# Kernel optimization log

Measured on AMD Instinct MI355X. Metric: run time of the kernel, lower is better.

The kernel has to match this reference:

```python
import jax, jax.numpy as jnp
import numpy as np

B, S, HID, NH, MAX_TOKENS = 2, 2048, 2048, 16, 2048
HD = HID // NH

def rotate_half(x):
    x1, x2 = x[..., :x.shape[-1] // 2], x[..., x.shape[-1] // 2:]
    return jnp.concatenate((-x2, x1), axis=-1)

def rope_tables():
    inv_freq = 1.0 / (10000.0 ** (jnp.arange(0, HD, 2, dtype=jnp.float32) / HD))
    t = jnp.arange(MAX_TOKENS, dtype=jnp.float32)
    freqs = jnp.outer(t, inv_freq)                       # [T, HD/2]
    emb = jnp.concatenate((freqs, freqs), axis=-1)       # [T, HD]
    return jnp.cos(emb), jnp.sin(emb)

def setup_inputs() -> dict:
    key = jax.random.key(0)
    ks = jax.random.split(key, 5)
    hidden_states = jax.random.normal(ks[0], (B, S, HID), dtype=jnp.float32)
    # additive causal mask [B, 1, S, S]: 0 on/below diag, large negative above
    neg = jnp.finfo(jnp.float32).min
    causal = jnp.where(jnp.tril(jnp.ones((S, S), dtype=bool)), 0.0, neg)
    attention_mask = jnp.broadcast_to(causal[None, None], (B, 1, S, S)).astype(jnp.float32)
    position_ids = jnp.broadcast_to(jnp.arange(S, dtype=jnp.int32), (B, S))
    scale = 1.0 / np.sqrt(HID)
    Wq = jax.random.normal(ks[1], (HID, HID), dtype=jnp.float32) * scale
    Wk = jax.random.normal(ks[2], (HID, HID), dtype=jnp.float32) * scale
    Wv = jax.random.normal(ks[3], (HID, HID), dtype=jnp.float32) * scale
    Wo = jax.random.normal(ks[4], (HID, HID), dtype=jnp.float32) * scale
    return {"hidden_states": hidden_states, "attention_mask": attention_mask,
            "position_ids": position_ids, "Wq": Wq, "Wk": Wk, "Wv": Wv, "Wo": Wo}

def reference(hidden_states, attention_mask, position_ids, Wq, Wk, Wv, Wo):
    b, s, _ = hidden_states.shape
    def proj(W):  # torch Linear: x @ W.T -> [b, H, s, hd]
        return (hidden_states @ W.T).reshape(b, s, NH, HD).transpose(0, 2, 1, 3)
    q, k, v = proj(Wq), proj(Wk), proj(Wv)
    cos_t, sin_t = rope_tables()
    cos = cos_t[position_ids][:, None]   # [b, 1, s, hd]
    sin = sin_t[position_ids][:, None]
    q = q * cos + rotate_half(q) * sin
    k = k * cos + rotate_half(k) * sin
    scores = jnp.einsum('bhqd,bhkd->bhqk', q, k) / np.sqrt(HD)
    scores = jnp.maximum(scores + attention_mask, jnp.finfo(scores.dtype).min)
    attn = jax.nn.softmax(scores.astype(jnp.float32), axis=-1).astype(q.dtype)
    out = jnp.einsum('bhqk,bhkd->bhqd', attn, v)
    out = out.transpose(0, 2, 1, 3).reshape(b, s, HID)
    return out @ Wo.T
```

## Files before the change

### kernel.cpp

```cpp
#include <hip/hip_runtime.h>

#define B_   2
#define S_   2048
#define HID_ 2048
#define NH_  16
#define HD_  128
#define MAXTOK_ 2048

typedef float  f32x4  __attribute__((ext_vector_type(4)));
typedef __bf16 bf16x8 __attribute__((ext_vector_type(8)));

__device__ __forceinline__ unsigned short f2bf(float f) {
  union { float fv; unsigned u; } v; v.fv = f;
  unsigned r = v.u + 0x7FFFu + ((v.u >> 16) & 1u);
  return (unsigned short)(r >> 16);
}
__device__ __forceinline__ float bf2f(unsigned short h) {
  union { unsigned u; float fv; } v; v.u = ((unsigned)h) << 16;
  return v.fv;
}

__device__ __forceinline__ void gload16(const void* g, void* lds) {
  __builtin_amdgcn_global_load_lds(
      (const __attribute__((address_space(1))) void*)g,
      (__attribute__((address_space(3))) void*)lds, 16, 0, 0);
}

#define H4_ (B_ * S_ * HID_ / 4)
#define W4_ (HID_ * HID_ / 4)
__global__ void cast_all(const float* __restrict__ h,  const float* __restrict__ wq,
                         const float* __restrict__ wk, const float* __restrict__ wv,
                         const float* __restrict__ wo,
                         unsigned short* __restrict__ xb,  unsigned short* __restrict__ wqb,
                         unsigned short* __restrict__ wkb, unsigned short* __restrict__ wvb,
                         unsigned short* __restrict__ wob) {
  const int total = H4_ + 4 * W4_;
  int i = blockIdx.x * blockDim.x + threadIdx.x;
  int stride = gridDim.x * blockDim.x;
  for (; i < total; i += stride) {
    const float* src; unsigned short* dst; int j;
    if (i < H4_) { src = h; dst = xb; j = i; }
    else {
      int k = i - H4_, wsel = k >> 20;
      j = k & (W4_ - 1);
      src = (wsel == 0) ? wq : (wsel == 1) ? wk : (wsel == 2) ? wv : wo;
      dst = (wsel == 0) ? wqb : (wsel == 1) ? wkb : (wsel == 2) ? wvb : wob;
    }
    float4 v = ((const float4*)src)[j];
    ushort4 o;
    o.x = f2bf(v.x); o.y = f2bf(v.y); o.z = f2bf(v.z); o.w = f2bf(v.w);
    ((ushort4*)dst)[j] = o;
  }
}

#define QKV_STG(gp, lp, rb) gload16((gp) + (size_t)(rb) * 2048, (lp) + (rb) * 64)

#define QKV_LOADA(MH) do { \
  _Pragma("unroll") \
  for (int mi_ = 0; mi_ < 4; ++mi_) { \
    const char* rp_ = (const char*)Acur + (size_t)((wm + (MH) * 64 + mi_ * 16 + rowq) * 128); \
    af[mi_][0] = *(const bf16x8*)(rp_ + cb0); \
    af[mi_][1] = *(const bf16x8*)(rp_ + cb1); \
  } } while (0)

#define QKV_LOADB(NP) do { \
  _Pragma("unroll") \
  for (int ni_ = 0; ni_ < 2; ++ni_) { \
    const char* rp_ = (const char*)Bcur + (size_t)((wn + (NP) * 32 + ni_ * 16 + rowq) * 128); \
    bfr[(NP) * 2 + ni_][0] = *(const bf16x8*)(rp_ + cb0); \
    bfr[(NP) * 2 + ni_][1] = *(const bf16x8*)(rp_ + cb1); \
  } } while (0)

#define QKV_MFMA(MH, NP) do { \
  _Pragma("unroll") \
  for (int mi_ = 0; mi_ < 4; ++mi_) { \
    _Pragma("unroll") \
    for (int ni_ = 0; ni_ < 2; ++ni_) { \
      f32x4 c_ = acc[(MH) * 4 + mi_][(NP) * 2 + ni_]; \
      c_ = __builtin_amdgcn_mfma_f32_16x16x32_bf16(af[mi_][0], bfr[(NP) * 2 + ni_][0], c_, 0, 0, 0); \
      c_ = __builtin_amdgcn_mfma_f32_16x16x32_bf16(af[mi_][1], bfr[(NP) * 2 + ni_][1], c_, 0, 0, 0); \
      acc[(MH) * 4 + mi_][(NP) * 2 + ni_] = c_; \
    } } } while (0)

#define QKV_BAR    asm volatile("s_barrier" ::: "memory")
#define QKV_VMC4   asm volatile("s_waitcnt vmcnt(4)" ::: "memory")
#define QKV_VMC2   asm volatile("s_waitcnt vmcnt(2)" ::: "memory")
#define QKV_VMC0   asm volatile("s_waitcnt vmcnt(0)" ::: "memory")

__global__ __launch_bounds__(512, 2)
void gemm_qkv(const unsigned short* __restrict__ A,
              const unsigned short* __restrict__ Bw,
              unsigned short* __restrict__ Qb,
              unsigned short* __restrict__ Kb,
              unsigned short* __restrict__ Vtmp) {
  const int K = HID_;
  const int NT = K / 64;
  __shared__ __align__(16) unsigned short As[2][256 * 64];
  __shared__ __align__(16) unsigned short Bs[2][256 * 64];

  const int tid = threadIdx.x, lane = tid & 63, w = tid >> 6;
  const int n0 = blockIdx.x * 256, m0 = blockIdx.y * 256;
  const int wm = (w >> 2) * 128, wn = (w & 3) * 64;
  const int rowq = lane & 15, klane = lane >> 4;
  const int sw  = (rowq & 7) << 4;
  const int cb0 = (klane * 16) ^ sw;
  const int cb1 = ((klane + 4) * 16) ^ sw;
  const int srow = tid >> 3;
  const int dc8  = (tid & 7) * 8;
  const int scol = (((tid & 7) * 16) ^ ((srow & 7) << 4)) >> 1;

  const unsigned short* Ag = A  + (size_t)(m0 + srow) * K + scol;
  const unsigned short* Bg = Bw + (size_t)(n0 + srow) * K + scol;

  f32x4 acc[8][4];
#pragma unroll
  for (int i = 0; i < 8; ++i)
#pragma unroll
    for (int j = 0; j < 4; ++j)
#pragma unroll
      for (int r = 0; r < 4; ++r) acc[i][j][r] = 0.f;

  bf16x8 af[4][2], bfr[4][2];

  {
    unsigned short* Al = (unsigned short*)&As[0][0] + srow * 64 + dc8;
    unsigned short* Bl = (unsigned short*)&Bs[0][0] + srow * 64 + dc8;
    QKV_STG(Bg, Bl, 0); QKV_STG(Bg, Bl, 64); QKV_STG(Bg, Bl, 128); QKV_STG(Bg, Bl, 192);
    QKV_STG(Ag, Al, 0); QKV_STG(Ag, Al, 128); QKV_STG(Ag, Al, 64); QKV_STG(Ag, Al, 192);
  }
  QKV_VMC2;
  QKV_BAR;

  const unsigned short* Acur = &As[0][0];
  const unsigned short* Bcur = &Bs[0][0];
  unsigned short* Anx = (unsigned short*)&As[1][0];
  unsigned short* Bnx = (unsigned short*)&Bs[1][0];

  for (int t = 0; t < NT - 1; ++t) {
    const int kn = (t + 1) * 64;
    const unsigned short* Agk = Ag + kn;
    const unsigned short* Bgk = Bg + kn;
    unsigned short* Al = Anx + srow * 64 + dc8;
    unsigned short* Bl = Bnx + srow * 64 + dc8;

    QKV_LOADA(0); QKV_LOADB(0);
    QKV_STG(Bgk, Bl, 0); QKV_STG(Bgk, Bl, 64);
    QKV_BAR;
    __builtin_amdgcn_s_setprio(1); QKV_MFMA(0, 0); __builtin_amdgcn_s_setprio(0);
    QKV_BAR;
    QKV_LOADB(1);
    QKV_STG(Bgk, Bl, 128); QKV_STG(Bgk, Bl, 192);
    QKV_BAR;
    __builtin_amdgcn_s_setprio(1); QKV_MFMA(0, 1); __builtin_amdgcn_s_setprio(0);
    QKV_VMC4;
    QKV_BAR;
    QKV_LOADA(1);
    QKV_STG(Agk, Al, 0); QKV_STG(Agk, Al, 128);
    QKV_BAR;
    __builtin_amdgcn_s_setprio(1); QKV_MFMA(1, 1); __builtin_amdgcn_s_setprio(0);
    QKV_BAR;
    QKV_STG(Agk, Al, 64); QKV_STG(Agk, Al, 192);
    QKV_BAR;
    __builtin_amdgcn_s_setprio(1); QKV_MFMA(1, 0); __builtin_amdgcn_s_setprio(0);
    QKV_VMC2;
    QKV_BAR;

    { const unsigned short* tp = Acur; Acur = Anx; Anx = (unsigned short*)tp; }
    { const unsigned short* tp = Bcur; Bcur = Bnx; Bnx = (unsigned short*)tp; }
  }

  QKV_LOADA(0); QKV_LOADB(0);
  QKV_BAR;
  __builtin_amdgcn_s_setprio(1); QKV_MFMA(0, 0); __builtin_amdgcn_s_setprio(0);
  QKV_BAR;
  QKV_LOADB(1);
  QKV_BAR;
  __builtin_amdgcn_s_setprio(1); QKV_MFMA(0, 1); __builtin_amdgcn_s_setprio(0);
  QKV_VMC0;
  QKV_BAR;
  QKV_LOADA(1);
  QKV_BAR;
  __builtin_amdgcn_s_setprio(1); QKV_MFMA(1, 1); __builtin_amdgcn_s_setprio(0);
  QKV_BAR;
  __builtin_amdgcn_s_setprio(1); QKV_MFMA(1, 0); __builtin_amdgcn_s_setprio(0);

  const int lr0 = klane * 4;
#pragma unroll
  for (int mi = 0; mi < 8; ++mi)
#pragma unroll
    for (int ni = 0; ni < 4; ++ni)
#pragma unroll
      for (int r = 0; r < 4; ++r) {
        int r_ = m0 + wm + mi * 16 + lr0 + r;
        int c_ = n0 + wn + ni * 16 + rowq;
        float v = acc[mi][ni][r];
        int b = r_ >> 11, s = r_ & 2047;
        int proj = c_ >> 11, cin = c_ & 2047;
        if (proj == 2) {
          Vtmp[(size_t)(b * S_ + s) * HID_ + cin] = f2bf(v);
        } else {
          int hh = cin >> 7, d = cin & 127;
          unsigned short* dst = (proj == 0) ? Qb : Kb;
          dst[(((size_t)(b * NH_ + hh) * S_ + s) * HD_) + d] = f2bf(v);
        }
      }
}

__global__ __launch_bounds__(256, 2)
void gemm_out(const unsigned short* __restrict__ A,
              const unsigned short* __restrict__ Bw,
              float* __restrict__ Cout) {
  const int N = HID_, K = HID_;
  __shared__ __align__(16) unsigned short As[128 * 32];
  __shared__ __align__(16) unsigned short Bs[128 * 32];
  const int tid = threadIdx.x, lane = tid & 63, w = tid >> 6;
  const int n0 = blockIdx.x * 128, m0 = blockIdx.y * 128;
  const int wm = (w & 1) * 64, wn = (w >> 1) * 64;
  const int rowq = lane & 15;
  const int klane = lane >> 4;
  const int ko = ((klane ^ ((rowq >> 1) & 3)) * 8);
  const int lr0 = klane * 4;

  f32x4 acc[4][4];
  for (int i = 0; i < 4; ++i)
    for (int j = 0; j < 4; ++j)
      for (int r = 0; r < 4; ++r) acc[i][j][r] = 0.f;

  for (int k0 = 0; k0 < K; k0 += 32) {
    __syncthreads();
    for (int c = 0; c < 2; ++c) {
      int chunk = (w * 2 + c) * 64 + lane;
      int row = chunk >> 2, cc = chunk & 3;
      int sc = (cc ^ ((row >> 1) & 3)) * 8;
      gload16(A + (size_t)(m0 + row) * K + k0 + sc, As + (w * 2 + c) * 512);
      gload16(Bw + (size_t)(n0 + row) * K + k0 + sc, Bs + (w * 2 + c) * 512);
    }
    __syncthreads();
    bf16x8 af[4], bfv[4];
    for (int i = 0; i < 4; ++i) {
      af[i]  = *(const bf16x8*)&As[(wm + i * 16 + rowq) * 32 + ko];
      bfv[i] = *(const bf16x8*)&Bs[(wn + i * 16 + rowq) * 32 + ko];
    }
    for (int mi = 0; mi < 4; ++mi)
      for (int ni = 0; ni < 4; ++ni)
        acc[mi][ni] = __builtin_amdgcn_mfma_f32_16x16x32_bf16(af[mi], bfv[ni], acc[mi][ni], 0, 0, 0);
  }

  for (int mi = 0; mi < 4; ++mi)
    for (int ni = 0; ni < 4; ++ni)
      for (int r = 0; r < 4; ++r) {
        int r_ = m0 + wm + mi * 16 + lr0 + r;
        int c_ = n0 + wn + ni * 16 + rowq;
        Cout[(size_t)r_ * N + c_] = acc[mi][ni][r];
      }
}

__global__ void rope_table(float2* __restrict__ tbl) {
  int i = blockIdx.x * blockDim.x + threadIdx.x;
  if (i >= MAXTOK_ * 64) return;
  int p = i >> 6, d = i & 63;
  float f = __expf(-(float)d * (9.210340371976184f / 64.f));
  float sn, cs;
  __sincosf((float)p * f, &sn, &cs);
  tbl[i] = make_float2(cs, sn);
}

#define QSCALE_ 0.12751744f
__global__ __launch_bounds__(256)
void rope_apply(unsigned short* __restrict__ Qb, unsigned short* __restrict__ Kb,
                const int* __restrict__ pos_ids, const float2* __restrict__ tbl) {
  int i = blockIdx.x * blockDim.x + threadIdx.x;
  int d = i & 63, bhs = i >> 6;
  int s = bhs & (S_ - 1);
  int b = bhs >> 15;
  int p = pos_ids[b * S_ + s];
  float2 cssn = tbl[p * 64 + d];
  size_t base = (size_t)bhs * HD_;
  {
    float x1 = bf2f(Qb[base + d]), x2 = bf2f(Qb[base + d + 64]);
    Qb[base + d]      = f2bf((x1 * cssn.x - x2 * cssn.y) * QSCALE_);
    Qb[base + d + 64] = f2bf((x2 * cssn.x + x1 * cssn.y) * QSCALE_);
  }
  {
    float x1 = bf2f(Kb[base + d]), x2 = bf2f(Kb[base + d + 64]);
    Kb[base + d]      = f2bf(x1 * cssn.x - x2 * cssn.y);
    Kb[base + d + 64] = f2bf(x2 * cssn.x + x1 * cssn.y);
  }
}

__global__ __launch_bounds__(256)
void transpose_v(const unsigned short* __restrict__ Vin,
                 unsigned short* __restrict__ Vt) {
  __shared__ unsigned short t[64 * 66];
  const int s0 = blockIdx.x * 64, d0 = blockIdx.y * 64, bh = blockIdx.z;
  const int b = bh >> 4, h = bh & 15;
  for (int it = 0; it < 16; ++it) {
    int lin = it * 256 + threadIdx.x;
    int sl = lin >> 6, dl = lin & 63;
    t[sl * 66 + dl] = Vin[(size_t)(b * S_ + s0 + sl) * HID_ + h * HD_ + d0 + dl];
  }
  __syncthreads();
  for (int it = 0; it < 16; ++it) {
    int lin = it * 256 + threadIdx.x;
    int dl = lin >> 6, sl = lin & 63;
    Vt[((size_t)bh * HD_ + d0 + dl) * S_ + s0 + sl] = t[sl * 66 + dl];
  }
}

#define KS_LD 136
#define VS_LD 72
#define PS_LD 72
__global__ __launch_bounds__(256, 2)
void attn_fused(const unsigned short* __restrict__ Qb,
                const unsigned short* __restrict__ Kb,
                const unsigned short* __restrict__ Vt,
                unsigned short* __restrict__ Ob) {
  __shared__ __align__(16) unsigned short Ks[64 * KS_LD];
  __shared__ __align__(16) unsigned short Vts[128 * VS_LD];
  __shared__ __align__(16) unsigned short Ps[4 * 16 * PS_LD];

  const int tid = threadIdx.x, lane = tid & 63, w = tid >> 6;
  const int bh = blockIdx.x;
  const int qt = (gridDim.y - 1) - blockIdx.y;
  const int q0 = qt * 64;
  const int b = bh >> 4, h = bh & 15;
  const int rowq = lane & 15;
  const int koff = (lane >> 4) * 8;
  const int lr0 = (lane >> 4) * 4;
  const size_t qkbase = (size_t)bh * (S_ * HD_);
  const size_t vbase  = (size_t)bh * (HD_ * S_);

  bf16x8 qf0, qf1, qf2, qf3;
  {
    const unsigned short* qrow = Qb + qkbase + (size_t)(q0 + w * 16 + rowq) * HD_;
    qf0 = *(const bf16x8*)(qrow + 0 * 32 + koff);
    qf1 = *(const bf16x8*)(qrow + 1 * 32 + koff);
    qf2 = *(const bf16x8*)(qrow + 2 * 32 + koff);
    qf3 = *(const bf16x8*)(qrow + 3 * 32 + koff);
  }

  const int krow = tid >> 4, kcol = (tid & 15) * 8;
  const int vrow = tid >> 3, vcol = (tid & 7) * 8;
  const unsigned short* kptr = Kb + qkbase + (size_t)krow * HD_ + kcol;
  const unsigned short* vptr = Vt + vbase + (size_t)vrow * S_ + vcol;

  f32x4 oacc[8];
  for (int i = 0; i < 8; ++i)
    for (int r = 0; r < 4; ++r) oacc[i][r] = 0.f;
  float m_r[4] = {-3e38f, -3e38f, -3e38f, -3e38f};
  float l_r[4] = {0.f, 0.f, 0.f, 0.f};

  const int nkt = qt + 1;

  float4 k0, k1, k2, k3, v0, v1, v2, v3;
  k0 = *(const float4*)(kptr + 0 * 16 * HD_);
  k1 = *(const float4*)(kptr + 1 * 16 * HD_);
  k2 = *(const float4*)(kptr + 2 * 16 * HD_);
  k3 = *(const float4*)(kptr + 3 * 16 * HD_);
  v0 = *(const float4*)(vptr + 0 * 32 * S_);
  v1 = *(const float4*)(vptr + 1 * 32 * S_);
  v2 = *(const float4*)(vptr + 2 * 32 * S_);
  v3 = *(const float4*)(vptr + 3 * 32 * S_);

  for (int kt = 0; kt < nkt; ++kt) {
    __syncthreads();
    *(float4*)&Ks[(krow + 0 * 16) * KS_LD + kcol] = k0;
    *(float4*)&Ks[(krow + 1 * 16) * KS_LD + kcol] = k1;
    *(float4*)&Ks[(krow + 2 * 16) * KS_LD + kcol] = k2;
    *(float4*)&Ks[(krow + 3 * 16) * KS_LD + kcol] = k3;
    *(float4*)&Vts[(vrow + 0 * 32) * VS_LD + vcol] = v0;
    *(float4*)&Vts[(vrow + 1 * 32) * VS_LD + vcol] = v1;
    *(float4*)&Vts[(vrow + 2 * 32) * VS_LD + vcol] = v2;
    *(float4*)&Vts[(vrow + 3 * 32) * VS_LD + vcol] = v3;
    if (kt + 1 < nkt) {
      const unsigned short* kp = kptr + (size_t)(kt + 1) * 64 * HD_;
      k0 = *(const float4*)(kp + 0 * 16 * HD_);
      k1 = *(const float4*)(kp + 1 * 16 * HD_);
      k2 = *(const float4*)(kp + 2 * 16 * HD_);
      k3 = *(const float4*)(kp + 3 * 16 * HD_);
    }
    __syncthreads();

    f32x4 sacc[4];
    for (int n = 0; n < 4; ++n)
      for (int r = 0; r < 4; ++r) sacc[n][r] = 0.f;
#pragma unroll
    for (int n = 0; n < 4; ++n) {
      const unsigned short* krow_p = &Ks[(n * 16 + rowq) * KS_LD + koff];
      sacc[n] = __builtin_amdgcn_mfma_f32_16x16x32_bf16(qf0, *(const bf16x8*)(krow_p + 0 * 32), sacc[n], 0, 0, 0);
      sacc[n] = __builtin_amdgcn_mfma_f32_16x16x32_bf16(qf1, *(const bf16x8*)(krow_p + 1 * 32), sacc[n], 0, 0, 0);
      sacc[n] = __builtin_amdgcn_mfma_f32_16x16x32_bf16(qf2, *(const bf16x8*)(krow_p + 2 * 32), sacc[n], 0, 0, 0);
      sacc[n] = __builtin_amdgcn_mfma_f32_16x16x32_bf16(qf3, *(const bf16x8*)(krow_p + 3 * 32), sacc[n], 0, 0, 0);
    }

    float tmax[4] = {-3e38f, -3e38f, -3e38f, -3e38f};
    if (kt == qt) {
      for (int n = 0; n < 4; ++n) {
        int col = n * 16 + rowq;
        for (int r = 0; r < 4; ++r) {
          int row = w * 16 + lr0 + r;
          float x = (col <= row) ? sacc[n][r] : -1e30f;
          sacc[n][r] = x;
          tmax[r] = fmaxf(tmax[r], x);
        }
      }
    } else {
      for (int n = 0; n < 4; ++n)
        for (int r = 0; r < 4; ++r)
          tmax[r] = fmaxf(tmax[r], sacc[n][r]);
    }
    for (int off = 1; off < 16; off <<= 1)
      for (int r = 0; r < 4; ++r) tmax[r] = fmaxf(tmax[r], __shfl_xor(tmax[r], off));
    float alpha[4];
    for (int r = 0; r < 4; ++r) {
      float mn = fmaxf(m_r[r], tmax[r]);
      alpha[r] = __builtin_amdgcn_exp2f(m_r[r] - mn);
      m_r[r] = mn;
    }
    float rs[4] = {0.f, 0.f, 0.f, 0.f};
    for (int n = 0; n < 4; ++n)
      for (int r = 0; r < 4; ++r) {
        float p = __builtin_amdgcn_exp2f(sacc[n][r] - m_r[r]);
        sacc[n][r] = p;
        rs[r] += p;
      }
    for (int off = 1; off < 16; off <<= 1)
      for (int r = 0; r < 4; ++r) rs[r] += __shfl_xor(rs[r], off);
    for (int r = 0; r < 4; ++r) l_r[r] = l_r[r] * alpha[r] + rs[r];
    for (int nd = 0; nd < 8; ++nd)
      for (int r = 0; r < 4; ++r) oacc[nd][r] *= alpha[r];

    if (kt + 1 < nkt) {
      const unsigned short* vp = vptr + (size_t)(kt + 1) * 64;
      v0 = *(const float4*)(vp + 0 * 32 * S_);
      v1 = *(const float4*)(vp + 1 * 32 * S_);
      v2 = *(const float4*)(vp + 2 * 32 * S_);
      v3 = *(const float4*)(vp + 3 * 32 * S_);
    }

    unsigned short* pw = &Ps[w * 16 * PS_LD];
    for (int n = 0; n < 4; ++n)
      for (int r = 0; r < 4; ++r)
        pw[(lr0 + r) * PS_LD + n * 16 + rowq] = f2bf(sacc[n][r]);

#pragma unroll
    for (int t2 = 0; t2 < 2; ++t2) {
      bf16x8 pa = *(const bf16x8*)&pw[rowq * PS_LD + t2 * 32 + koff];
      for (int nd = 0; nd < 8; ++nd) {
        bf16x8 vb = *(const bf16x8*)&Vts[(nd * 16 + rowq) * VS_LD + t2 * 32 + koff];
        oacc[nd] = __builtin_amdgcn_mfma_f32_16x16x32_bf16(pa, vb, oacc[nd], 0, 0, 0);
      }
    }
  }

  float linv[4];
  for (int r = 0; r < 4; ++r) linv[r] = __builtin_amdgcn_rcpf(l_r[r]);
  for (int nd = 0; nd < 8; ++nd) {
    int col = h * HD_ + nd * 16 + rowq;
    for (int r = 0; r < 4; ++r) {
      int row = q0 + w * 16 + lr0 + r;
      Ob[(size_t)(b * S_ + row) * HID_ + col] = f2bf(oacc[nd][r] * linv[r]);
    }
  }
}

extern "C" void kernel_launch(void* const* d_in, const int* in_sizes, int n_in,
                              void* d_out, int out_size, void* d_ws, size_t ws_size,
                              hipStream_t stream) {
  (void)in_sizes; (void)n_in; (void)out_size; (void)ws_size;
  const float* hidden = (const float*)d_in[0];
  const int* pos = (const int*)d_in[2];
  const float* Wq = (const float*)d_in[3];
  const float* Wk = (const float*)d_in[4];
  const float* Wv = (const float*)d_in[5];
  const float* Wo = (const float*)d_in[6];
  float* out = (float*)d_out;

  char* ws = (char*)d_ws;
  unsigned short* Xb   = (unsigned short*)(ws);
  unsigned short* Wqb  = (unsigned short*)(ws + 16777216);
  unsigned short* Wkb  = (unsigned short*)(ws + 25165824);
  unsigned short* Wvb  = (unsigned short*)(ws + 33554432);
  unsigned short* Wob  = (unsigned short*)(ws + 41943040);
  unsigned short* Qb   = (unsigned short*)(ws + 50331648);
  unsigned short* Kb   = (unsigned short*)(ws + 67108864);
  unsigned short* Vtmp = (unsigned short*)(ws + 83886080);
  unsigned short* Vtb  = (unsigned short*)(ws + 100663296);
  unsigned short* Ob   = Xb;
  float2* tbl          = (float2*)ws;

  cast_all<<<2048, 256, 0, stream>>>(hidden, Wq, Wk, Wv, Wo, Xb, Wqb, Wkb, Wvb, Wob);

  dim3 gq(3 * HID_ / 256, (B_ * S_) / 256);
  gemm_qkv<<<gq, 512, 0, stream>>>(Xb, Wqb, Qb, Kb, Vtmp);

  rope_table<<<(MAXTOK_ * 64) / 256, 256, 0, stream>>>(tbl);
  rope_apply<<<(B_ * NH_ * S_ * 64) / 256, 256, 0, stream>>>(Qb, Kb, pos, tbl);

  dim3 tg(S_ / 64, HD_ / 64, B_ * NH_);
  transpose_v<<<tg, 256, 0, stream>>>(Vtmp, Vtb);

  dim3 ag(B_ * NH_, S_ / 64);
  attn_fused<<<ag, 256, 0, stream>>>(Qb, Kb, Vtb, Ob);

  dim3 go(HID_ / 128, (B_ * S_) / 128);
  gemm_out<<<go, 256, 0, stream>>>(Ob, Wob, out);
}
```

Before: 415.2 us.

## Shrink QKV GEMM tile N to 192 to fill more CUs

Changes the fused QKV GEMM block tile from 256x256 to 256x192 and each wave's subtile to 128x48. The grid grows from 24x16 to 32x16 blocks, which fills the GPU's compute units more evenly. The inner k-loop is reorganised into four A-quarter MFMA phases with three B fragments held in registers, and the staging schedule is rebalanced for the smaller B tile. The cost is lower arithmetic intensity per block, and the wait-count and barrier choreography must still match the new load order.

```diff
diff --git a/kernel.cpp b/kernel.cpp
--- a/kernel.cpp
+++ b/kernel.cpp
@@ -55,31 +55,31 @@
 
 #define QKV_STG(gp, lp, rb) gload16((gp) + (size_t)(rb) * 2048, (lp) + (rb) * 64)
 
-#define QKV_LOADA(MH) do { \
+#define QKV_LOADA(Q) do { \
   _Pragma("unroll") \
-  for (int mi_ = 0; mi_ < 4; ++mi_) { \
-    const char* rp_ = (const char*)Acur + (size_t)((wm + (MH) * 64 + mi_ * 16 + rowq) * 128); \
+  for (int mi_ = 0; mi_ < 2; ++mi_) { \
+    const char* rp_ = (const char*)Acur + (size_t)((wm + (Q) * 32 + mi_ * 16 + rowq) * 128); \
     af[mi_][0] = *(const bf16x8*)(rp_ + cb0); \
     af[mi_][1] = *(const bf16x8*)(rp_ + cb1); \
   } } while (0)
 
-#define QKV_LOADB(NP) do { \
+#define QKV_LOADB() do { \
   _Pragma("unroll") \
-  for (int ni_ = 0; ni_ < 2; ++ni_) { \
-    const char* rp_ = (const char*)Bcur + (size_t)((wn + (NP) * 32 + ni_ * 16 + rowq) * 128); \
-    bfr[(NP) * 2 + ni_][0] = *(const bf16x8*)(rp_ + cb0); \
-    bfr[(NP) * 2 + ni_][1] = *(const bf16x8*)(rp_ + cb1); \
+  for (int ni_ = 0; ni_ < 3; ++ni_) { \
+    const char* rp_ = (const char*)Bcur + (size_t)((wn + ni_ * 16 + rowq) * 128); \
+    bfr[ni_][0] = *(const bf16x8*)(rp_ + cb0); \
+    bfr[ni_][1] = *(const bf16x8*)(rp_ + cb1); \
   } } while (0)
 
-#define QKV_MFMA(MH, NP) do { \
+#define QKV_MFMA(Q) do { \
   _Pragma("unroll") \
-  for (int mi_ = 0; mi_ < 4; ++mi_) { \
+  for (int mi_ = 0; mi_ < 2; ++mi_) { \
     _Pragma("unroll") \
-    for (int ni_ = 0; ni_ < 2; ++ni_) { \
-      f32x4 c_ = acc[(MH) * 4 + mi_][(NP) * 2 + ni_]; \
-      c_ = __builtin_amdgcn_mfma_f32_16x16x32_bf16(af[mi_][0], bfr[(NP) * 2 + ni_][0], c_, 0, 0, 0); \
-      c_ = __builtin_amdgcn_mfma_f32_16x16x32_bf16(af[mi_][1], bfr[(NP) * 2 + ni_][1], c_, 0, 0, 0); \
-      acc[(MH) * 4 + mi_][(NP) * 2 + ni_] = c_; \
+    for (int ni_ = 0; ni_ < 3; ++ni_) { \
+      f32x4 c_ = acc[(Q) * 2 + mi_][ni_]; \
+      c_ = __builtin_amdgcn_mfma_f32_16x16x32_bf16(af[mi_][0], bfr[ni_][0], c_, 0, 0, 0); \
+      c_ = __builtin_amdgcn_mfma_f32_16x16x32_bf16(af[mi_][1], bfr[ni_][1], c_, 0, 0, 0); \
+      acc[(Q) * 2 + mi_][ni_] = c_; \
     } } } while (0)
 
 #define QKV_BAR    asm volatile("s_barrier" ::: "memory")
@@ -96,11 +96,11 @@
   const int K = HID_;
   const int NT = K / 64;
   __shared__ __align__(16) unsigned short As[2][256 * 64];
-  __shared__ __align__(16) unsigned short Bs[2][256 * 64];
+  __shared__ __align__(16) unsigned short Bs[2][192 * 64];
 
   const int tid = threadIdx.x, lane = tid & 63, w = tid >> 6;
-  const int n0 = blockIdx.x * 256, m0 = blockIdx.y * 256;
-  const int wm = (w >> 2) * 128, wn = (w & 3) * 64;
+  const int n0 = blockIdx.x * 192, m0 = blockIdx.y * 256;
+  const int wm = (w >> 2) * 128, wn = (w & 3) * 48;
   const int rowq = lane & 15, klane = lane >> 4;
   const int sw  = (rowq & 7) << 4;
   const int cb0 = (klane * 16) ^ sw;
@@ -112,21 +112,22 @@
   const unsigned short* Ag = A  + (size_t)(m0 + srow) * K + scol;
   const unsigned short* Bg = Bw + (size_t)(n0 + srow) * K + scol;
 
-  f32x4 acc[8][4];
+  f32x4 acc[8][3];
 #pragma unroll
   for (int i = 0; i < 8; ++i)
 #pragma unroll
-    for (int j = 0; j < 4; ++j)
+    for (int j = 0; j < 3; ++j)
 #pragma unroll
       for (int r = 0; r < 4; ++r) acc[i][j][r] = 0.f;
 
-  bf16x8 af[4][2], bfr[4][2];
+  bf16x8 af[2][2], bfr[3][2];
 
   {
     unsigned short* Al = (unsigned short*)&As[0][0] + srow * 64 + dc8;
     unsigned short* Bl = (unsigned short*)&Bs[0][0] + srow * 64 + dc8;
-    QKV_STG(Bg, Bl, 0); QKV_STG(Bg, Bl, 64); QKV_STG(Bg, Bl, 128); QKV_STG(Bg, Bl, 192);
-    QKV_STG(Ag, Al, 0); QKV_STG(Ag, Al, 128); QKV_STG(Ag, Al, 64); QKV_STG(Ag, Al, 192);
+    QKV_STG(Bg, Bl, 0); QKV_STG(Bg, Bl, 64); QKV_STG(Bg, Bl, 128);
+    QKV_STG(Ag, Al, 0); QKV_STG(Ag, Al, 128);
+    QKV_STG(Ag, Al, 64); QKV_STG(Ag, Al, 192);
   }
   QKV_VMC2;
   QKV_BAR;
@@ -143,25 +144,26 @@
     unsigned short* Al = Anx + srow * 64 + dc8;
     unsigned short* Bl = Bnx + srow * 64 + dc8;
 
-    QKV_LOADA(0); QKV_LOADB(0);
+    QKV_LOADA(0); QKV_LOADB();
     QKV_STG(Bgk, Bl, 0); QKV_STG(Bgk, Bl, 64);
     QKV_BAR;
-    __builtin_amdgcn_s_setprio(1); QKV_MFMA(0, 0); __builtin_amdgcn_s_setprio(0);
-    QKV_BAR;
-    QKV_LOADB(1);
-    QKV_STG(Bgk, Bl, 128); QKV_STG(Bgk, Bl, 192);
-    QKV_BAR;
-    __builtin_amdgcn_s_setprio(1); QKV_MFMA(0, 1); __builtin_amdgcn_s_setprio(0);
+    __builtin_amdgcn_s_setprio(1); QKV_MFMA(0); __builtin_amdgcn_s_setprio(0);
+    QKV_BAR;
+    QKV_LOADA(1);
+    QKV_STG(Bgk, Bl, 128); QKV_STG(Agk, Al, 0);
+    QKV_BAR;
+    __builtin_amdgcn_s_setprio(1); QKV_MFMA(1); __builtin_amdgcn_s_setprio(0);
     QKV_VMC4;
     QKV_BAR;
-    QKV_LOADA(1);
-    QKV_STG(Agk, Al, 0); QKV_STG(Agk, Al, 128);
-    QKV_BAR;
-    __builtin_amdgcn_s_setprio(1); QKV_MFMA(1, 1); __builtin_amdgcn_s_setprio(0);
-    QKV_BAR;
-    QKV_STG(Agk, Al, 64); QKV_STG(Agk, Al, 192);
-    QKV_BAR;
-    __builtin_amdgcn_s_setprio(1); QKV_MFMA(1, 0); __builtin_amdgcn_s_setprio(0);
+    QKV_LOADA(2);
+    QKV_STG(Agk, Al, 128); QKV_STG(Agk, Al, 64);
+    QKV_BAR;
+    __builtin_amdgcn_s_setprio(1); QKV_MFMA(2); __builtin_amdgcn_s_setprio(0);
+    QKV_BAR;
+    QKV_LOADA(3);
+    QKV_STG(Agk, Al, 192);
+    QKV_BAR;
+    __builtin_amdgcn_s_setprio(1); QKV_MFMA(3); __builtin_amdgcn_s_setprio(0);
     QKV_VMC2;
     QKV_BAR;
 
@@ -169,26 +171,27 @@
     { const unsigned short* tp = Bcur; Bcur = Bnx; Bnx = (unsigned short*)tp; }
   }
 
-  QKV_LOADA(0); QKV_LOADB(0);
-  QKV_BAR;
-  __builtin_amdgcn_s_setprio(1); QKV_MFMA(0, 0); __builtin_amdgcn_s_setprio(0);
-  QKV_BAR;
-  QKV_LOADB(1);
-  QKV_BAR;
-  __builtin_amdgcn_s_setprio(1); QKV_MFMA(0, 1); __builtin_amdgcn_s_setprio(0);
+  QKV_LOADA(0); QKV_LOADB();
+  QKV_BAR;
+  __builtin_amdgcn_s_setprio(1); QKV_MFMA(0); __builtin_amdgcn_s_setprio(0);
+  QKV_BAR;
+  QKV_LOADA(1);
+  QKV_BAR;
+  __builtin_amdgcn_s_setprio(1); QKV_MFMA(1); __builtin_amdgcn_s_setprio(0);
   QKV_VMC0;
   QKV_BAR;
-  QKV_LOADA(1);
-  QKV_BAR;
-  __builtin_amdgcn_s_setprio(1); QKV_MFMA(1, 1); __builtin_amdgcn_s_setprio(0);
-  QKV_BAR;
-  __builtin_amdgcn_s_setprio(1); QKV_MFMA(1, 0); __builtin_amdgcn_s_setprio(0);
+  QKV_LOADA(2);
+  QKV_BAR;
+  __builtin_amdgcn_s_setprio(1); QKV_MFMA(2); __builtin_amdgcn_s_setprio(0);
+  QKV_BAR;
+  QKV_LOADA(3);
+  __builtin_amdgcn_s_setprio(1); QKV_MFMA(3); __builtin_amdgcn_s_setprio(0);
 
   const int lr0 = klane * 4;
 #pragma unroll
   for (int mi = 0; mi < 8; ++mi)
 #pragma unroll
-    for (int ni = 0; ni < 4; ++ni)
+    for (int ni = 0; ni < 3; ++ni)
 #pragma unroll
       for (int r = 0; r < 4; ++r) {
         int r_ = m0 + wm + mi * 16 + lr0 + r;
@@ -491,7 +494,7 @@
 
   cast_all<<<2048, 256, 0, stream>>>(hidden, Wq, Wk, Wv, Wo, Xb, Wqb, Wkb, Wvb, Wob);
 
-  dim3 gq(3 * HID_ / 256, (B_ * S_) / 256);
+  dim3 gq(3 * HID_ / 192, (B_ * S_) / 256);
   gemm_qkv<<<gq, 512, 0, stream>>>(Xb, Wqb, Qb, Kb, Vtmp);
 
   rope_table<<<(MAXTOK_ * 64) / 256, 256, 0, stream>>>(tbl);
```

Result: faster. 399.9 us (-3.7%).
